# Optimization experiments

Measured on AMD Instinct MI355X. Metric: run time of the kernel, lower is better.

## Reference

```python
import jax, jax.numpy as jnp
import numpy as np

BIN = 256      # bin_num
DELTA = 0.01   # Huber delta
IM = 256       # imSize


def _soft_hist(u):
    # u: [B,H,W] values in [0,1]; BiasedConv1 with weight=1, bias_k = -(-1 + 2k/BIN)
    bias = 1.0 - 2.0 * jnp.arange(BIN, dtype=u.dtype) / BIN          # [BIN]
    a1 = u[:, None, :, :] + bias[None, :, None, None]                # [B,BIN,H,W]
    return jax.nn.relu(1.0 - jnp.abs(a1) * (BIN - 1))                # triangular kernel


def _hist2d(img):
    # img: [B,2,H,W] in [-1,1]
    ha = _soft_hist((img[:, 0] + 1.0) / 2.0)                         # [B,BIN,H,W]
    hb = _soft_hist((img[:, 1] + 1.0) / 2.0)                         # [B,BIN,H,W]
    H, W = img.shape[2], img.shape[3]
    # torch: repeat/repeat-view + elementwise mul + AvgPool2d(imSize)
    # == per-pixel outer product of (hb, ha) averaged over all pixels:
    # hist2d[b, j, r] = mean_hw hb[b,j,h,w] * ha[b,r,h,w]
    h2 = jnp.einsum('bjhw,brhw->bjr', hb, ha) / (H * W)              # [B,BIN,BIN]
    return h2[:, None]                                               # [B,1,BIN,BIN]


def reference(inp_image, ref_image):
    h_inp = _hist2d(inp_image)
    h_gt = _hist2d(ref_image)
    mann = jnp.abs(h_inp - h_gt)
    eucl = 0.5 * mann ** 2
    mask = (mann < DELTA).astype(mann.dtype)
    loss = eucl * mask / DELTA + (mann - 0.5 * DELTA) * (1.0 - mask)
    return jnp.sum(loss, axis=1, keepdims=True)                      # [B,1,BIN,BIN]


def setup_inputs() -> dict:
    key = jax.random.key(0)
    k1, k2 = jax.random.split(key)
    inp = jax.random.uniform(k1, (2, 2, IM, IM), dtype=jnp.float32) * 2.0 - 1.0
    ref = jax.random.uniform(k2, (2, 2, IM, IM), dtype=jnp.float32) * 2.0 - 1.0
    return {"inp_image": inp, "ref_image": ref}
```

## Files before the change

kernel.cpp:

```cpp
#include <hip/hip_runtime.h>


#define NPIX 65536
#define BINS 256

__global__ void zero_kernel(float4* __restrict__ p) {
    int i = blockIdx.x * blockDim.x + threadIdx.x;
    p[i] = make_float4(0.f, 0.f, 0.f, 0.f);
}

__global__ void hist_kernel(const float* __restrict__ inp,
                            const float* __restrict__ ref,
                            float* __restrict__ hist) {
    int gid = blockIdx.x * blockDim.x + threadIdx.x;
    int pix = gid & (NPIX - 1);
    int bb  = (gid >> 16) & 1;
    int im  = gid >> 17;
    const float* src = im ? ref : inp;
    float x0 = src[bb * (2 * NPIX) + pix];
    float x1 = src[bb * (2 * NPIX) + NPIX + pix];
    float* h = hist + (im * 2 + bb) * (BINS * BINS);

    float t0 = 64.f * x0 + 192.f;
    float t1 = 64.f * x1 + 192.f;
    int k0 = (int)floorf(t0);
    int k1 = (int)floorf(t1);

    float wr[2]; int ir[2]; int nr = 0;
    #pragma unroll
    for (int d = 0; d < 2; ++d) {
        int k = k0 + d;
        float w = 1.f - fabsf(t0 - (float)k) * 1.9921875f;
        if (w > 0.f && k >= 0 && k < BINS) { wr[nr] = w; ir[nr] = k; ++nr; }
    }
    float wj[2]; int ij[2]; int nj = 0;
    #pragma unroll
    for (int d = 0; d < 2; ++d) {
        int k = k1 + d;
        float w = 1.f - fabsf(t1 - (float)k) * 1.9921875f;
        if (w > 0.f && k >= 0 && k < BINS) { wj[nj] = w; ij[nj] = k; ++nj; }
    }
    for (int a = 0; a < nj; ++a)
        for (int b = 0; b < nr; ++b)
            atomicAdd(&h[ij[a] * BINS + ir[b]], wj[a] * wr[b]);
}

__global__ void loss_kernel(const float* __restrict__ hist,
                            float* __restrict__ out) {
    int idx = blockIdx.x * blockDim.x + threadIdx.x;
    int bb = idx >> 16;
    int jr = idx & (NPIX - 1);
    const float inv = 1.f / 65536.f;
    float h1 = hist[(0 * 2 + bb) * (BINS * BINS) + jr] * inv;
    float h2 = hist[(1 * 2 + bb) * (BINS * BINS) + jr] * inv;
    float mann = fabsf(h1 - h2);
    float loss = (mann < 0.01f) ? (50.f * mann * mann) : (mann - 0.005f);
    out[idx] = loss;
}

extern "C" void kernel_launch(void* const* d_in, const int* in_sizes, int n_in,
                              void* d_out, int out_size, void* d_ws, size_t ws_size,
                              hipStream_t stream) {
    const float* inp = (const float*)d_in[0];
    const float* ref = (const float*)d_in[1];
    float* hist = (float*)d_ws;
    float* out  = (float*)d_out;

    zero_kernel<<<(4 * NPIX / 4) / 256, 256, 0, stream>>>((float4*)hist);
    hist_kernel<<<(4 * NPIX) / 256, 256, 0, stream>>>(inp, ref, hist);
    loss_kernel<<<(2 * NPIX) / 256, 256, 0, stream>>>(hist, out);
}
```

Before: 71.90 us.

## Fuse zero, histogram and loss kernels into one cooperative launch with grid sync

Replaces three separate kernel launches with a single cooperative kernel of 256 blocks that zeroes the histogram, accumulates it with atomics, and computes the Huber loss, separated by grid-wide syncs. Each thread now handles four pixels and two outputs. The aim is to remove launch overhead and inter-kernel gaps. In exchange it adds grid-sync cost and runs far fewer threads in flight for the atomic phase, which may reduce latency hiding.

```diff
diff --git a/kernel.cpp b/kernel.cpp
--- a/kernel.cpp
+++ b/kernel.cpp
@@ -1,61 +1,73 @@
 #include <hip/hip_runtime.h>
+#include <hip/hip_cooperative_groups.h>
+
+namespace cg = cooperative_groups;
 
 
 #define NPIX 65536
 #define BINS 256
 
-__global__ void zero_kernel(float4* __restrict__ p) {
-    int i = blockIdx.x * blockDim.x + threadIdx.x;
-    p[i] = make_float4(0.f, 0.f, 0.f, 0.f);
-}
+__global__ void __launch_bounds__(256)
+fused_kernel(const float* __restrict__ inp,
+             const float* __restrict__ ref,
+             float* __restrict__ hist,
+             float* __restrict__ out) {
+    cg::grid_group grid = cg::this_grid();
+    int tid = blockIdx.x * blockDim.x + threadIdx.x;
 
-__global__ void hist_kernel(const float* __restrict__ inp,
-                            const float* __restrict__ ref,
-                            float* __restrict__ hist) {
-    int gid = blockIdx.x * blockDim.x + threadIdx.x;
-    int pix = gid & (NPIX - 1);
-    int bb  = (gid >> 16) & 1;
-    int im  = gid >> 17;
-    const float* src = im ? ref : inp;
-    float x0 = src[bb * (2 * NPIX) + pix];
-    float x1 = src[bb * (2 * NPIX) + NPIX + pix];
-    float* h = hist + (im * 2 + bb) * (BINS * BINS);
+    ((float4*)hist)[tid] = make_float4(0.f, 0.f, 0.f, 0.f);
+    __threadfence();
+    grid.sync();
 
-    float t0 = 64.f * x0 + 192.f;
-    float t1 = 64.f * x1 + 192.f;
-    int k0 = (int)floorf(t0);
-    int k1 = (int)floorf(t1);
+    #pragma unroll
+    for (int s = 0; s < 4; ++s) {
+        int gid = tid + s * NPIX;
+        int pix = gid & (NPIX - 1);
+        int bb  = (gid >> 16) & 1;
+        int im  = gid >> 17;
+        const float* src = im ? ref : inp;
+        float x0 = src[bb * (2 * NPIX) + pix];
+        float x1 = src[bb * (2 * NPIX) + NPIX + pix];
+        float* h = hist + (im * 2 + bb) * (BINS * BINS);
 
-    float wr[2]; int ir[2]; int nr = 0;
+        float t0 = 64.f * x0 + 192.f;
+        float t1 = 64.f * x1 + 192.f;
+        int k0 = (int)floorf(t0);
+        int k1 = (int)floorf(t1);
+
+        float wr[2]; int ir[2]; int nr = 0;
+        #pragma unroll
+        for (int d = 0; d < 2; ++d) {
+            int k = k0 + d;
+            float w = 1.f - fabsf(t0 - (float)k) * 1.9921875f;
+            if (w > 0.f && k >= 0 && k < BINS) { wr[nr] = w; ir[nr] = k; ++nr; }
+        }
+        float wj[2]; int ij[2]; int nj = 0;
+        #pragma unroll
+        for (int d = 0; d < 2; ++d) {
+            int k = k1 + d;
+            float w = 1.f - fabsf(t1 - (float)k) * 1.9921875f;
+            if (w > 0.f && k >= 0 && k < BINS) { wj[nj] = w; ij[nj] = k; ++nj; }
+        }
+        for (int a = 0; a < nj; ++a)
+            for (int b = 0; b < nr; ++b)
+                atomicAdd(&h[ij[a] * BINS + ir[b]], wj[a] * wr[b]);
+    }
+    __threadfence();
+    grid.sync();
+
     #pragma unroll
-    for (int d = 0; d < 2; ++d) {
-        int k = k0 + d;
-        float w = 1.f - fabsf(t0 - (float)k) * 1.9921875f;
-        if (w > 0.f && k >= 0 && k < BINS) { wr[nr] = w; ir[nr] = k; ++nr; }
+    for (int s = 0; s < 2; ++s) {
+        int idx = tid + s * NPIX;
+        int bb = idx >> 16;
+        int jr = idx & (NPIX - 1);
+        const float inv = 1.f / 65536.f;
+        float h1 = hist[(0 * 2 + bb) * (BINS * BINS) + jr] * inv;
+        float h2 = hist[(1 * 2 + bb) * (BINS * BINS) + jr] * inv;
+        float mann = fabsf(h1 - h2);
+        float loss = (mann < 0.01f) ? (50.f * mann * mann) : (mann - 0.005f);
+        out[idx] = loss;
     }
-    float wj[2]; int ij[2]; int nj = 0;
-    #pragma unroll
-    for (int d = 0; d < 2; ++d) {
-        int k = k1 + d;
-        float w = 1.f - fabsf(t1 - (float)k) * 1.9921875f;
-        if (w > 0.f && k >= 0 && k < BINS) { wj[nj] = w; ij[nj] = k; ++nj; }
-    }
-    for (int a = 0; a < nj; ++a)
-        for (int b = 0; b < nr; ++b)
-            atomicAdd(&h[ij[a] * BINS + ir[b]], wj[a] * wr[b]);
-}
-
-__global__ void loss_kernel(const float* __restrict__ hist,
-                            float* __restrict__ out) {
-    int idx = blockIdx.x * blockDim.x + threadIdx.x;
-    int bb = idx >> 16;
-    int jr = idx & (NPIX - 1);
-    const float inv = 1.f / 65536.f;
-    float h1 = hist[(0 * 2 + bb) * (BINS * BINS) + jr] * inv;
-    float h2 = hist[(1 * 2 + bb) * (BINS * BINS) + jr] * inv;
-    float mann = fabsf(h1 - h2);
-    float loss = (mann < 0.01f) ? (50.f * mann * mann) : (mann - 0.005f);
-    out[idx] = loss;
 }
 
 extern "C" void kernel_launch(void* const* d_in, const int* in_sizes, int n_in,
@@ -66,7 +78,7 @@
     float* hist = (float*)d_ws;
     float* out  = (float*)d_out;
 
-    zero_kernel<<<(4 * NPIX / 4) / 256, 256, 0, stream>>>((float4*)hist);
-    hist_kernel<<<(4 * NPIX) / 256, 256, 0, stream>>>(inp, ref, hist);
-    loss_kernel<<<(2 * NPIX) / 256, 256, 0, stream>>>(hist, out);
+    void* args[] = { (void*)&inp, (void*)&ref, (void*)&hist, (void*)&out };
+    hipLaunchCooperativeKernel((void*)fused_kernel, dim3(256), dim3(256),
+                               args, 0, stream);
 }
```

Result: slower. 168.2 us (+134.0%).

## Replicate histograms across blocks to spread atomic contention, reduce in loss kernel

Applied to the files above, without the earlier changes.

Makes 8 replicated copies of the four 256x256 histograms in the workspace. Each scatter block writes into the copy picked by its block index, and each thread now handles 4 pixels with a 256-block grid. The loss kernel sums the 8 replicas before computing the Huber loss. The goal is to cut global atomic contention on hot bins. The cost is 8x more memory to zero and read back, and fewer threads doing the scatter.

```diff
diff --git a/kernel.cpp b/kernel.cpp
--- a/kernel.cpp
+++ b/kernel.cpp
@@ -3,57 +3,74 @@
 
 #define NPIX 65536
 #define BINS 256
+#define REPL 8
+#define HSZ  (4 * NPIX)
 
-__global__ void zero_kernel(float4* __restrict__ p) {
-    int i = blockIdx.x * blockDim.x + threadIdx.x;
-    p[i] = make_float4(0.f, 0.f, 0.f, 0.f);
+__global__ void __launch_bounds__(256)
+zero_kernel(float4* __restrict__ hist4) {
+    int tid = blockIdx.x * blockDim.x + threadIdx.x;
+    #pragma unroll
+    for (int r = 0; r < REPL; ++r)
+        hist4[tid + r * (HSZ / 4)] = make_float4(0.f, 0.f, 0.f, 0.f);
 }
 
-__global__ void hist_kernel(const float* __restrict__ inp,
-                            const float* __restrict__ ref,
-                            float* __restrict__ hist) {
-    int gid = blockIdx.x * blockDim.x + threadIdx.x;
-    int pix = gid & (NPIX - 1);
-    int bb  = (gid >> 16) & 1;
-    int im  = gid >> 17;
-    const float* src = im ? ref : inp;
-    float x0 = src[bb * (2 * NPIX) + pix];
-    float x1 = src[bb * (2 * NPIX) + NPIX + pix];
-    float* h = hist + (im * 2 + bb) * (BINS * BINS);
+__global__ void __launch_bounds__(256)
+scatter_kernel(const float* __restrict__ inp,
+               const float* __restrict__ ref,
+               float* __restrict__ hist) {
+    int tid = blockIdx.x * blockDim.x + threadIdx.x;
+    float* hrep = hist + (blockIdx.x & (REPL - 1)) * HSZ;
 
-    float t0 = 64.f * x0 + 192.f;
-    float t1 = 64.f * x1 + 192.f;
-    int k0 = (int)floorf(t0);
-    int k1 = (int)floorf(t1);
+    #pragma unroll
+    for (int s = 0; s < 4; ++s) {
+        int gid = tid + s * NPIX;
+        int pix = gid & (NPIX - 1);
+        int bb  = (gid >> 16) & 1;
+        int im  = gid >> 17;
+        const float* src = im ? ref : inp;
+        float x0 = src[bb * (2 * NPIX) + pix];
+        float x1 = src[bb * (2 * NPIX) + NPIX + pix];
+        float* h = hrep + (im * 2 + bb) * (BINS * BINS);
 
-    float wr[2]; int ir[2]; int nr = 0;
-    #pragma unroll
-    for (int d = 0; d < 2; ++d) {
-        int k = k0 + d;
-        float w = 1.f - fabsf(t0 - (float)k) * 1.9921875f;
-        if (w > 0.f && k >= 0 && k < BINS) { wr[nr] = w; ir[nr] = k; ++nr; }
+        float t0 = 64.f * x0 + 192.f;
+        float t1 = 64.f * x1 + 192.f;
+        int k0 = (int)floorf(t0);
+        int k1 = (int)floorf(t1);
+
+        float wr[2]; int ir[2]; int nr = 0;
+        #pragma unroll
+        for (int d = 0; d < 2; ++d) {
+            int k = k0 + d;
+            float w = 1.f - fabsf(t0 - (float)k) * 1.9921875f;
+            if (w > 0.f && k >= 0 && k < BINS) { wr[nr] = w; ir[nr] = k; ++nr; }
+        }
+        float wj[2]; int ij[2]; int nj = 0;
+        #pragma unroll
+        for (int d = 0; d < 2; ++d) {
+            int k = k1 + d;
+            float w = 1.f - fabsf(t1 - (float)k) * 1.9921875f;
+            if (w > 0.f && k >= 0 && k < BINS) { wj[nj] = w; ij[nj] = k; ++nj; }
+        }
+        for (int a = 0; a < nj; ++a)
+            for (int b = 0; b < nr; ++b)
+                atomicAdd(&h[ij[a] * BINS + ir[b]], wj[a] * wr[b]);
     }
-    float wj[2]; int ij[2]; int nj = 0;
-    #pragma unroll
-    for (int d = 0; d < 2; ++d) {
-        int k = k1 + d;
-        float w = 1.f - fabsf(t1 - (float)k) * 1.9921875f;
-        if (w > 0.f && k >= 0 && k < BINS) { wj[nj] = w; ij[nj] = k; ++nj; }
-    }
-    for (int a = 0; a < nj; ++a)
-        for (int b = 0; b < nr; ++b)
-            atomicAdd(&h[ij[a] * BINS + ir[b]], wj[a] * wr[b]);
 }
 
-__global__ void loss_kernel(const float* __restrict__ hist,
-                            float* __restrict__ out) {
+__global__ void __launch_bounds__(256)
+loss_kernel(const float* __restrict__ hist,
+            float* __restrict__ out) {
     int idx = blockIdx.x * blockDim.x + threadIdx.x;
     int bb = idx >> 16;
     int jr = idx & (NPIX - 1);
+    float s_inp = 0.f, s_ref = 0.f;
+    #pragma unroll
+    for (int r = 0; r < REPL; ++r) {
+        s_inp += hist[r * HSZ + (0 * 2 + bb) * (BINS * BINS) + jr];
+        s_ref += hist[r * HSZ + (1 * 2 + bb) * (BINS * BINS) + jr];
+    }
     const float inv = 1.f / 65536.f;
-    float h1 = hist[(0 * 2 + bb) * (BINS * BINS) + jr] * inv;
-    float h2 = hist[(1 * 2 + bb) * (BINS * BINS) + jr] * inv;
-    float mann = fabsf(h1 - h2);
+    float mann = fabsf(s_inp - s_ref) * inv;
     float loss = (mann < 0.01f) ? (50.f * mann * mann) : (mann - 0.005f);
     out[idx] = loss;
 }
@@ -66,7 +83,7 @@
     float* hist = (float*)d_ws;
     float* out  = (float*)d_out;
 
-    zero_kernel<<<(4 * NPIX / 4) / 256, 256, 0, stream>>>((float4*)hist);
-    hist_kernel<<<(4 * NPIX) / 256, 256, 0, stream>>>(inp, ref, hist);
+    zero_kernel<<<256, 256, 0, stream>>>((float4*)hist);
+    scatter_kernel<<<256, 256, 0, stream>>>(inp, ref, hist);
     loss_kernel<<<(2 * NPIX) / 256, 256, 0, stream>>>(hist, out);
 }
```

Result: slower. 75.15 us (+4.5%).

## Replicate histograms to cut atomic contention and fold zeroing into loss kernel

Applied to the files above, without the earlier changes.

The scatter kernel now spreads atomics across four histogram replicas, chosen by block index, to reduce contention on the same bins. The loss kernel sums the replicas, computes the Huber loss, and writes zeros back into the workspace. This removes the separate zero kernel launch. The cost is a four-times larger workspace and four times the reads in the loss pass. Correctness now depends on the workspace starting zeroed and persisting between calls.

```diff
diff --git a/kernel.cpp b/kernel.cpp
--- a/kernel.cpp
+++ b/kernel.cpp
@@ -3,15 +3,13 @@
 
 #define NPIX 65536
 #define BINS 256
+#define REPL 4
+#define HSZ  (4 * NPIX)
 
-__global__ void zero_kernel(float4* __restrict__ p) {
-    int i = blockIdx.x * blockDim.x + threadIdx.x;
-    p[i] = make_float4(0.f, 0.f, 0.f, 0.f);
-}
-
-__global__ void hist_kernel(const float* __restrict__ inp,
-                            const float* __restrict__ ref,
-                            float* __restrict__ hist) {
+__global__ void __launch_bounds__(256)
+scatter_kernel(const float* __restrict__ inp,
+               const float* __restrict__ ref,
+               float* __restrict__ hist) {
     int gid = blockIdx.x * blockDim.x + threadIdx.x;
     int pix = gid & (NPIX - 1);
     int bb  = (gid >> 16) & 1;
@@ -19,7 +17,8 @@
     const float* src = im ? ref : inp;
     float x0 = src[bb * (2 * NPIX) + pix];
     float x1 = src[bb * (2 * NPIX) + NPIX + pix];
-    float* h = hist + (im * 2 + bb) * (BINS * BINS);
+    float* h = hist + (blockIdx.x & (REPL - 1)) * HSZ
+                    + (im * 2 + bb) * (BINS * BINS);
 
     float t0 = 64.f * x0 + 192.f;
     float t1 = 64.f * x1 + 192.f;
@@ -45,15 +44,24 @@
             atomicAdd(&h[ij[a] * BINS + ir[b]], wj[a] * wr[b]);
 }
 
-__global__ void loss_kernel(const float* __restrict__ hist,
-                            float* __restrict__ out) {
+__global__ void __launch_bounds__(256)
+loss_rezero_kernel(float* __restrict__ hist,
+                   float* __restrict__ out) {
     int idx = blockIdx.x * blockDim.x + threadIdx.x;
     int bb = idx >> 16;
     int jr = idx & (NPIX - 1);
+    float s_inp = 0.f, s_ref = 0.f;
+    #pragma unroll
+    for (int r = 0; r < REPL; ++r) {
+        float* pi = &hist[r * HSZ + (0 * 2 + bb) * (BINS * BINS) + jr];
+        float* pr = &hist[r * HSZ + (1 * 2 + bb) * (BINS * BINS) + jr];
+        s_inp += *pi;
+        s_ref += *pr;
+        *pi = 0.f;
+        *pr = 0.f;
+    }
     const float inv = 1.f / 65536.f;
-    float h1 = hist[(0 * 2 + bb) * (BINS * BINS) + jr] * inv;
-    float h2 = hist[(1 * 2 + bb) * (BINS * BINS) + jr] * inv;
-    float mann = fabsf(h1 - h2);
+    float mann = fabsf(s_inp - s_ref) * inv;
     float loss = (mann < 0.01f) ? (50.f * mann * mann) : (mann - 0.005f);
     out[idx] = loss;
 }
@@ -66,7 +74,6 @@
     float* hist = (float*)d_ws;
     float* out  = (float*)d_out;
 
-    zero_kernel<<<(4 * NPIX / 4) / 256, 256, 0, stream>>>((float4*)hist);
-    hist_kernel<<<(4 * NPIX) / 256, 256, 0, stream>>>(inp, ref, hist);
-    loss_kernel<<<(2 * NPIX) / 256, 256, 0, stream>>>(hist, out);
+    scatter_kernel<<<(4 * NPIX) / 256, 256, 0, stream>>>(inp, ref, hist);
+    loss_rezero_kernel<<<(2 * NPIX) / 256, 256, 0, stream>>>(hist, out);
 }
```

Result: no change. 71.13 us (-1.1%).
